# Kernel optimization log

Measured on AMD Instinct MI355X. Metric: run time of the kernel, lower is better.

The kernel has to match this reference:

```python
import jax, jax.numpy as jnp
import numpy as np

B, D, K, H, E, Z = 64, 25000, 16, 128, 256, 32


def setup_inputs() -> dict:
    key = jax.random.key(0)
    ks = jax.random.split(key, 10)
    s = 0.02
    return {
        "x": jax.random.normal(ks[0], (B, D), jnp.float32),
        "mask": jax.random.randint(ks[1], (B, D), 0, 2, jnp.int32),
        "feat_emb": jax.random.normal(ks[2], (D, K), jnp.float32),          # feature_embedding [D,K]
        "feat_bias": jnp.zeros((D, 1), jnp.float32),                        # feature_bias [D,1]
        "W1": jax.random.normal(ks[3], (1 + K + 1, H), jnp.float32) * s,    # h_layer linear 1 (in,out)
        "b1": jnp.zeros((H,), jnp.float32),
        "W2": jax.random.normal(ks[4], (H, K), jnp.float32) * s,            # h_layer linear 2
        "b2": jnp.zeros((K,), jnp.float32),
        "We1": jax.random.normal(ks[5], (K, E), jnp.float32) * s,           # encoder_mlp linear 1
        "be1": jnp.zeros((E,), jnp.float32),
        "We2": jax.random.normal(ks[6], (E, 2 * Z), jnp.float32) * s,       # encoder_mlp linear 2
        "be2": jnp.zeros((2 * Z,), jnp.float32),
    }


def reference(x, mask, feat_emb, feat_bias, W1, b1, W2, b2, We1, be1, We2, be2):
    b, d = x.shape
    k = feat_emb.shape[1]
    # Build per-(sample, feature) input rows: [x_bd, F_d(K), bias_d] -> [B, D, 1+K+1]
    h_in = jnp.concatenate(
        [
            x[:, :, None],
            jnp.broadcast_to(feat_emb[None, :, :], (b, d, k)),
            jnp.broadcast_to(feat_bias[None, :, :], (b, d, 1)),
        ],
        axis=-1,
    )
    # Shared small MLP (h_layer), dropout is identity at rate 0.0
    h = jax.nn.relu(h_in @ W1 + b1)          # [B, D, H]
    h = jax.nn.relu(h @ W2 + b2)             # [B, D, K]
    # Masked sum pooling over features
    c = jnp.sum(h * mask.astype(h.dtype)[:, :, None], axis=1)  # [B, K]
    # encoder_mlp
    enc = jax.nn.relu(c @ We1 + be1) @ We2 + be2                # [B, 2Z]
    mu, logvar = jnp.split(enc, 2, axis=-1)
    return mu, logvar
```

## Files before the change

kernel.cpp:

```cpp
#include <hip/hip_runtime.h>
#include <hip/hip_bf16.h>

#define B 64
#define D 25000
#define K 16
#define H 128
#define E 256
#define Z 32
#define DTILE 25
#define XSTR 65
#define MSTR 68

typedef __attribute__((ext_vector_type(8))) short short8;
typedef __attribute__((ext_vector_type(4))) float f32x4;

__device__ __forceinline__ unsigned short f2bf(float f) {
    union { float f; unsigned u; } v; v.f = f;
    unsigned u = v.u + 0x7FFF + ((v.u >> 16) & 1);
    return (unsigned short)(u >> 16);
}
__device__ __forceinline__ float bf2f(unsigned short s) {
    union { unsigned u; float f; } v; v.u = (unsigned)s << 16;
    return v.f;
}

__global__ __launch_bounds__(256, 4) void partial_main_kernel(
    const float* __restrict__ x, const int* __restrict__ mask,
    const float* __restrict__ feat_emb, const float* __restrict__ feat_bias,
    const float* __restrict__ W1, const float* __restrict__ b1,
    const float* __restrict__ W2, const float* __restrict__ b2,
    float* __restrict__ c_out)
{
    __shared__ __align__(16) float sW1[18 * H];
    __shared__ __align__(16) float sG[DTILE * H];
    __shared__ __align__(16) float sFE[DTILE * K];
    __shared__ float sFB[DTILE];
    __shared__ __align__(16) float sX[DTILE * XSTR];
    __shared__ __align__(16) float sM[DTILE * MSTR];

    const int t    = threadIdx.x;
    const int d0   = blockIdx.x * DTILE;
    const int lane = t & 63;
    const int wv   = t >> 6;
    const int g    = lane >> 4;
    const int n    = lane & 15;

    for (int i = t; i < 18 * H; i += 256) sW1[i] = W1[i];
    for (int i = t; i < H * K;  i += 256) sG[i]  = W2[i];
    for (int i = t; i < DTILE * K; i += 256) sFE[i] = feat_emb[d0 * K + i];
    if (t < DTILE) sFB[t] = feat_bias[d0 + t];
    for (int i = t; i < DTILE * B; i += 256) {
        int bb = i / DTILE, dd = i - bb * DTILE;
        sX[dd * XSTR + bb] = x[bb * D + d0 + dd];
        sM[dd * MSTR + bb] = (float)mask[bb * D + d0 + dd];
    }
    __syncthreads();

    short8 Bf1[4], Bf2[4];
    #pragma unroll
    for (int s = 0; s < 4; ++s) {
        union { short8 v; unsigned short e[8]; } u1, u2;
        #pragma unroll
        for (int j = 0; j < 8; ++j) {
            int k = s * 32 + g * 8 + j;
            float w = sG[k * K + n];
            unsigned short hi = f2bf(w);
            u1.e[j] = hi;
            u2.e[j] = f2bf(w - bf2f(hi));
        }
        Bf1[s] = u1.v; Bf2[s] = u2.v;
    }
    float w0r[4][8];
    #pragma unroll
    for (int s = 0; s < 4; ++s) {
        const float4* wp = (const float4*)&sW1[s * 32 + g * 8];
        float4 a0 = wp[0], a1 = wp[1];
        w0r[s][0] = a0.x; w0r[s][1] = a0.y; w0r[s][2] = a0.z; w0r[s][3] = a0.w;
        w0r[s][4] = a1.x; w0r[s][5] = a1.y; w0r[s][6] = a1.z; w0r[s][7] = a1.w;
    }
    const float b2n = b2[n];
    __syncthreads();

    for (int i = t; i < DTILE * H; i += 256) {
        int dd = i >> 7, h = i & (H - 1);
        float acc = fmaf(sFB[dd], sW1[17 * H + h], b1[h]);
        #pragma unroll
        for (int k = 0; k < K; ++k)
            acc = fmaf(sFE[dd * K + k], sW1[(1 + k) * H + h], acc);
        sG[i] = acc;
    }
    __syncthreads();

    f32x4 cacc = {0.f, 0.f, 0.f, 0.f};
    const int xoff = wv * 16 + n;
    const int moff = wv * 16 + g * 4;

    for (int dd = 0; dd < DTILE; ++dd) {
        const float xv = sX[dd * XSTR + xoff];
        f32x4 c1 = {0.f, 0.f, 0.f, 0.f};
        f32x4 c2 = {0.f, 0.f, 0.f, 0.f};
        #pragma unroll
        for (int s = 0; s < 4; ++s) {
            const float4* gp = (const float4*)&sG[dd * H + s * 32 + g * 8];
            const float4 g0 = gp[0], g1 = gp[1];
            float h0 = fmaxf(fmaf(xv, w0r[s][0], g0.x), 0.f);
            float h1 = fmaxf(fmaf(xv, w0r[s][1], g0.y), 0.f);
            float h2 = fmaxf(fmaf(xv, w0r[s][2], g0.z), 0.f);
            float h3 = fmaxf(fmaf(xv, w0r[s][3], g0.w), 0.f);
            float h4 = fmaxf(fmaf(xv, w0r[s][4], g1.x), 0.f);
            float h5 = fmaxf(fmaf(xv, w0r[s][5], g1.y), 0.f);
            float h6 = fmaxf(fmaf(xv, w0r[s][6], g1.z), 0.f);
            float h7 = fmaxf(fmaf(xv, w0r[s][7], g1.w), 0.f);
            union { short8 v; unsigned u[4]; } a;
            union { __hip_bfloat162 h; unsigned u; } cv;
            cv.h = __float22bfloat162_rn(make_float2(h0, h1)); a.u[0] = cv.u;
            cv.h = __float22bfloat162_rn(make_float2(h2, h3)); a.u[1] = cv.u;
            cv.h = __float22bfloat162_rn(make_float2(h4, h5)); a.u[2] = cv.u;
            cv.h = __float22bfloat162_rn(make_float2(h6, h7)); a.u[3] = cv.u;
            c1 = __builtin_amdgcn_mfma_f32_16x16x32_bf16(a.v, Bf1[s], c1, 0, 0, 0);
            c2 = __builtin_amdgcn_mfma_f32_16x16x32_bf16(a.v, Bf2[s], c2, 0, 0, 0);
        }
        const float4 mv = *(const float4*)&sM[dd * MSTR + moff];
        float p0 = c1[0] + c2[0] + b2n;
        float p1 = c1[1] + c2[1] + b2n;
        float p2 = c1[2] + c2[2] + b2n;
        float p3 = c1[3] + c2[3] + b2n;
        cacc[0] = fmaf(mv.x, fmaxf(p0, 0.f), cacc[0]);
        cacc[1] = fmaf(mv.y, fmaxf(p1, 0.f), cacc[1]);
        cacc[2] = fmaf(mv.z, fmaxf(p2, 0.f), cacc[2]);
        cacc[3] = fmaf(mv.w, fmaxf(p3, 0.f), cacc[3]);
    }

    #pragma unroll
    for (int r = 0; r < 4; ++r)
        atomicAdd(&c_out[(moff + r) * K + n], cacc[r]);
}

__global__ __launch_bounds__(256) void partial_enc_kernel(
    const float* __restrict__ c, const float* __restrict__ We1,
    const float* __restrict__ be1, const float* __restrict__ We2,
    const float* __restrict__ be2, float* __restrict__ out)
{
    const int b = blockIdx.x;
    const int t = threadIdx.x;
    __shared__ float sc[K];
    __shared__ float st1[E];
    __shared__ float red[256];

    if (t < K) sc[t] = c[b * K + t];
    __syncthreads();

    {
        float acc = be1[t];
        #pragma unroll
        for (int k = 0; k < K; ++k)
            acc = fmaf(sc[k], We1[k * E + t], acc);
        st1[t] = fmaxf(acc, 0.f);
    }
    __syncthreads();

    const int j = t & 63, seg = t >> 6;
    float acc = 0.f;
    #pragma unroll 4
    for (int e = seg * 64; e < seg * 64 + 64; ++e)
        acc = fmaf(st1[e], We2[e * 64 + j], acc);
    red[t] = acc;
    __syncthreads();

    if (t < 64) {
        float v = red[j] + red[64 + j] + red[128 + j] + red[192 + j] + be2[j];
        if (j < Z) out[b * Z + j] = v;
        else       out[B * Z + b * Z + (j - Z)] = v;
    }
}

extern "C" void kernel_launch(void* const* d_in, const int* in_sizes, int n_in,
                              void* d_out, int out_size, void* d_ws, size_t ws_size,
                              hipStream_t stream) {
    const float* x         = (const float*)d_in[0];
    const int*   mask      = (const int*)  d_in[1];
    const float* feat_emb  = (const float*)d_in[2];
    const float* feat_bias = (const float*)d_in[3];
    const float* W1        = (const float*)d_in[4];
    const float* b1        = (const float*)d_in[5];
    const float* W2        = (const float*)d_in[6];
    const float* b2        = (const float*)d_in[7];
    const float* We1       = (const float*)d_in[8];
    const float* be1       = (const float*)d_in[9];
    const float* We2       = (const float*)d_in[10];
    const float* be2       = (const float*)d_in[11];

    float* c_ws = (float*)d_ws;
    hipMemsetAsync(c_ws, 0, B * K * sizeof(float), stream);

    partial_main_kernel<<<D / DTILE, 256, 0, stream>>>(
        x, mask, feat_emb, feat_bias, W1, b1, W2, b2, c_ws);
    partial_enc_kernel<<<B, 256, 0, stream>>>(
        c_ws, We1, be1, We2, be2, (float*)d_out);
}
```

Before: 133.0 us.

## Spread atomics over replicated accumulators, precompute split-bf16 W2, shrink tiles

```diff
diff --git a/kernel.cpp b/kernel.cpp
--- a/kernel.cpp
+++ b/kernel.cpp
@@ -7,9 +7,13 @@
 #define H 128
 #define E 256
 #define Z 32
-#define DTILE 25
+#define DTILE 10
+#define NBLK (D / DTILE)
+#define NREP 64
 #define XSTR 65
 #define MSTR 68
+
+#define REPF (NREP * B * K)
 
 typedef __attribute__((ext_vector_type(8))) short short8;
 typedef __attribute__((ext_vector_type(4))) float f32x4;
@@ -23,20 +27,42 @@
     union { unsigned u; float f; } v; v.u = (unsigned)s << 16;
     return v.f;
 }
-
-__global__ __launch_bounds__(256, 4) void partial_main_kernel(
+__device__ __forceinline__ unsigned cvt_pk_bf16(float a, float b) {
+    unsigned r;
+    asm("v_cvt_pk_bf16_f32 %0, %1, %2" : "=v"(r) : "v"(a), "v"(b));
+    return r;
+}
+
+__global__ __launch_bounds__(256) void prep_kernel(
+    const float* __restrict__ W2, float* __restrict__ rep,
+    unsigned short* __restrict__ hi, unsigned short* __restrict__ lo)
+{
+    const int t = threadIdx.x;
+    if (blockIdx.x == 0) {
+        for (int i = t; i < H * K; i += 256) {
+            int j = i & 7, n = (i >> 3) & 15, g = (i >> 7) & 3, s = i >> 9;
+            int k = s * 32 + g * 8 + j;
+            float w = W2[k * K + n];
+            unsigned short h = f2bf(w);
+            hi[i] = h;
+            lo[i] = f2bf(w - bf2f(h));
+        }
+    } else {
+        int r = blockIdx.x - 1;
+        for (int i = t; i < B * K; i += 256) rep[r * B * K + i] = 0.f;
+    }
+}
+
+__global__ __launch_bounds__(256, 8) void partial_main_kernel(
     const float* __restrict__ x, const int* __restrict__ mask,
     const float* __restrict__ feat_emb, const float* __restrict__ feat_bias,
     const float* __restrict__ W1, const float* __restrict__ b1,
-    const float* __restrict__ W2, const float* __restrict__ b2,
-    float* __restrict__ c_out)
+    const float* __restrict__ b2, float* __restrict__ rep,
+    const unsigned short* __restrict__ hi, const unsigned short* __restrict__ lo)
 {
-    __shared__ __align__(16) float sW1[18 * H];
     __shared__ __align__(16) float sG[DTILE * H];
-    __shared__ __align__(16) float sFE[DTILE * K];
-    __shared__ float sFB[DTILE];
     __shared__ __align__(16) float sX[DTILE * XSTR];
-    __shared__ __align__(16) float sM[DTILE * MSTR];
+    __shared__ __align__(16) float sMf[DTILE * MSTR];
 
     const int t    = threadIdx.x;
     const int d0   = blockIdx.x * DTILE;
@@ -45,50 +71,36 @@
     const int g    = lane >> 4;
     const int n    = lane & 15;
 
-    for (int i = t; i < 18 * H; i += 256) sW1[i] = W1[i];
-    for (int i = t; i < H * K;  i += 256) sG[i]  = W2[i];
-    for (int i = t; i < DTILE * K; i += 256) sFE[i] = feat_emb[d0 * K + i];
-    if (t < DTILE) sFB[t] = feat_bias[d0 + t];
     for (int i = t; i < DTILE * B; i += 256) {
         int bb = i / DTILE, dd = i - bb * DTILE;
-        sX[dd * XSTR + bb] = x[bb * D + d0 + dd];
-        sM[dd * MSTR + bb] = (float)mask[bb * D + d0 + dd];
-    }
-    __syncthreads();
+        sX[dd * XSTR + bb]  = x[bb * D + d0 + dd];
+        sMf[dd * MSTR + bb] = (float)mask[bb * D + d0 + dd];
+    }
+    for (int i = t; i < DTILE * H; i += 256) {
+        int dd = i >> 7, h = i & (H - 1);
+        int d = d0 + dd;
+        float acc = fmaf(feat_bias[d], W1[17 * H + h], b1[h]);
+        #pragma unroll
+        for (int k = 0; k < K; ++k)
+            acc = fmaf(feat_emb[d * K + k], W1[(1 + k) * H + h], acc);
+        sG[i] = acc;
+    }
 
     short8 Bf1[4], Bf2[4];
     #pragma unroll
     for (int s = 0; s < 4; ++s) {
-        union { short8 v; unsigned short e[8]; } u1, u2;
-        #pragma unroll
-        for (int j = 0; j < 8; ++j) {
-            int k = s * 32 + g * 8 + j;
-            float w = sG[k * K + n];
-            unsigned short hi = f2bf(w);
-            u1.e[j] = hi;
-            u2.e[j] = f2bf(w - bf2f(hi));
-        }
-        Bf1[s] = u1.v; Bf2[s] = u2.v;
+        Bf1[s] = *(const short8*)(hi + (((s * 4 + g) * 16 + n) << 3));
+        Bf2[s] = *(const short8*)(lo + (((s * 4 + g) * 16 + n) << 3));
     }
     float w0r[4][8];
     #pragma unroll
     for (int s = 0; s < 4; ++s) {
-        const float4* wp = (const float4*)&sW1[s * 32 + g * 8];
+        const float4* wp = (const float4*)&W1[s * 32 + g * 8];
         float4 a0 = wp[0], a1 = wp[1];
         w0r[s][0] = a0.x; w0r[s][1] = a0.y; w0r[s][2] = a0.z; w0r[s][3] = a0.w;
         w0r[s][4] = a1.x; w0r[s][5] = a1.y; w0r[s][6] = a1.z; w0r[s][7] = a1.w;
     }
     const float b2n = b2[n];
-    __syncthreads();
-
-    for (int i = t; i < DTILE * H; i += 256) {
-        int dd = i >> 7, h = i & (H - 1);
-        float acc = fmaf(sFB[dd], sW1[17 * H + h], b1[h]);
-        #pragma unroll
-        for (int k = 0; k < K; ++k)
-            acc = fmaf(sFE[dd * K + k], sW1[(1 + k) * H + h], acc);
-        sG[i] = acc;
-    }
     __syncthreads();
 
     f32x4 cacc = {0.f, 0.f, 0.f, 0.f};
@@ -112,15 +124,14 @@
             float h6 = fmaxf(fmaf(xv, w0r[s][6], g1.z), 0.f);
             float h7 = fmaxf(fmaf(xv, w0r[s][7], g1.w), 0.f);
             union { short8 v; unsigned u[4]; } a;
-            union { __hip_bfloat162 h; unsigned u; } cv;
-            cv.h = __float22bfloat162_rn(make_float2(h0, h1)); a.u[0] = cv.u;
-            cv.h = __float22bfloat162_rn(make_float2(h2, h3)); a.u[1] = cv.u;
-            cv.h = __float22bfloat162_rn(make_float2(h4, h5)); a.u[2] = cv.u;
-            cv.h = __float22bfloat162_rn(make_float2(h6, h7)); a.u[3] = cv.u;
+            a.u[0] = cvt_pk_bf16(h0, h1);
+            a.u[1] = cvt_pk_bf16(h2, h3);
+            a.u[2] = cvt_pk_bf16(h4, h5);
+            a.u[3] = cvt_pk_bf16(h6, h7);
             c1 = __builtin_amdgcn_mfma_f32_16x16x32_bf16(a.v, Bf1[s], c1, 0, 0, 0);
             c2 = __builtin_amdgcn_mfma_f32_16x16x32_bf16(a.v, Bf2[s], c2, 0, 0, 0);
         }
-        const float4 mv = *(const float4*)&sM[dd * MSTR + moff];
+        const float4 mv = *(const float4*)&sMf[dd * MSTR + moff];
         float p0 = c1[0] + c2[0] + b2n;
         float p1 = c1[1] + c2[1] + b2n;
         float p2 = c1[2] + c2[2] + b2n;
@@ -131,13 +142,14 @@
         cacc[3] = fmaf(mv.w, fmaxf(p3, 0.f), cacc[3]);
     }
 
+    float* crep = rep + (size_t)(blockIdx.x & (NREP - 1)) * (B * K);
     #pragma unroll
     for (int r = 0; r < 4; ++r)
-        atomicAdd(&c_out[(moff + r) * K + n], cacc[r]);
+        atomicAdd(&crep[(moff + r) * K + n], cacc[r]);
 }
 
 __global__ __launch_bounds__(256) void partial_enc_kernel(
-    const float* __restrict__ c, const float* __restrict__ We1,
+    const float* __restrict__ rep, const float* __restrict__ We1,
     const float* __restrict__ be1, const float* __restrict__ We2,
     const float* __restrict__ be2, float* __restrict__ out)
 {
@@ -147,7 +159,21 @@
     __shared__ float st1[E];
     __shared__ float red[256];
 
-    if (t < K) sc[t] = c[b * K + t];
+    {
+        const int k = t & 15, grp = t >> 4;
+        float a = 0.f;
+        #pragma unroll
+        for (int r = grp; r < NREP; r += 16)
+            a += rep[r * (B * K) + b * K + k];
+        red[t] = a;
+    }
+    __syncthreads();
+    if (t < K) {
+        float s2 = 0.f;
+        #pragma unroll
+        for (int q = 0; q < 16; ++q) s2 += red[q * 16 + t];
+        sc[t] = s2;
+    }
     __syncthreads();
 
     {
@@ -190,11 +216,13 @@
     const float* We2       = (const float*)d_in[10];
     const float* be2       = (const float*)d_in[11];
 
-    float* c_ws = (float*)d_ws;
-    hipMemsetAsync(c_ws, 0, B * K * sizeof(float), stream);
-
-    partial_main_kernel<<<D / DTILE, 256, 0, stream>>>(
-        x, mask, feat_emb, feat_bias, W1, b1, W2, b2, c_ws);
+    float* rep = (float*)d_ws;
+    unsigned short* hi = (unsigned short*)((char*)d_ws + (size_t)REPF * 4);
+    unsigned short* lo = hi + H * K;
+
+    prep_kernel<<<1 + NREP, 256, 0, stream>>>(W2, rep, hi, lo);
+    partial_main_kernel<<<NBLK, 256, 0, stream>>>(
+        x, mask, feat_emb, feat_bias, W1, b1, b2, rep, hi, lo);
     partial_enc_kernel<<<B, 256, 0, stream>>>(
-        c_ws, We1, be1, We2, be2, (float*)d_out);
-}
+        rep, We1, be1, We2, be2, (float*)d_out);
+}
```

New measurement: 256.6 us. 93.0% more time.
